# Kernel tuning notes

Measured on AMD Instinct MI355X. Metric: run time of the kernel, lower is better.

## Reference

```python
import jax, jax.numpy as jnp
import numpy as np

DIM = 192
NUM_HEADS = 6
KERNELS = [3, 5, 7]
DILATIONS = [1, 2, 3]
NBRANCH = 3
HEADS_B = NUM_HEADS // NBRANCH      # heads per branch = 2
HEAD_DIM = DIM // NUM_HEADS         # 32


def _axis_idx(L, K, d):
    """NATTEN-style neighborhood indices along one axis with dilation.
    Returns (nbr[L,K] absolute neighbor positions, bias[L,K] rpb indices in [0, 2K-2]).
    """
    i = np.arange(L)
    g = i % d                                 # dilation group
    ii = i // d                               # index within subgrid
    Lg = (L - g + d - 1) // d                 # subgrid length of each group
    start = np.clip(ii - K // 2, 0, Lg - K)   # clamp window inside bounds
    ki = np.arange(K)
    nbr = g[:, None] + (start[:, None] + ki[None, :]) * d        # [L,K]
    bias = start[:, None] + ki[None, :] - ii[:, None] + (K - 1)  # [L,K]
    return nbr, bias


def _branch(xb, K, d, rpb):
    # xb: [B,H,W, 3*heads*head_dim] laid out as (3, heads, head_dim)
    B, H, W, _ = xb.shape
    qkv = xb.reshape(B, H, W, 3, HEADS_B, HEAD_DIM).transpose(3, 0, 4, 1, 2, 5)
    q, k, v = qkv[0], qkv[1], qkv[2]          # [B,h,H,W,hd]
    q = q * (HEAD_DIM ** -0.5)
    nh, bh = _axis_idx(H, K, d)
    nw, bw = _axis_idx(W, K, d)
    # gather K x K neighborhoods: [B,h,H,W,K,K,hd]
    k_nb = k[:, :, nh[:, None, :, None], nw[None, :, None, :]]
    attn = jnp.einsum('bhijd,bhijkld->bhijkl', q, k_nb)
    attn = attn + rpb[:, bh[:, None, :, None], bw[None, :, None, :]][None]
    attn = jax.nn.softmax(attn.reshape(B, HEADS_B, H, W, K * K), axis=-1)
    attn = attn.reshape(B, HEADS_B, H, W, K, K)
    v_nb = v[:, :, nh[:, None, :, None], nw[None, :, None, :]]
    y = jnp.einsum('bhijkl,bhijkld->bhijd', attn, v_nb)
    return y.transpose(0, 2, 3, 1, 4).reshape(B, H, W, HEADS_B * HEAD_DIM)


def setup_inputs() -> dict:
    key = jax.random.key(0)
    ks = jax.random.split(key, 8)
    B, H, W = 8, 64, 64
    return {
        'x': jax.random.normal(ks[0], (B, DIM, H, W), jnp.float32),
        'qkv_w': jax.random.normal(ks[1], (3 * DIM, DIM), jnp.float32) * 0.02,
        'qkv_b': jnp.zeros((3 * DIM,), jnp.float32),
        'proj_w': jax.random.normal(ks[2], (DIM, DIM), jnp.float32) * 0.02,
        'proj_b': jnp.zeros((DIM,), jnp.float32),
        'rpb0': jax.random.normal(ks[3], (HEADS_B, 5, 5), jnp.float32) * 0.02,
        'rpb1': jax.random.normal(ks[4], (HEADS_B, 9, 9), jnp.float32) * 0.02,
        'rpb2': jax.random.normal(ks[5], (HEADS_B, 13, 13), jnp.float32) * 0.02,
    }


def reference(x, qkv_w, qkv_b, proj_w, proj_b, rpb0, rpb1, rpb2):
    # x: [B,C,H,W] -> BHWC
    xp = x.transpose(0, 2, 3, 1)
    qkv = xp @ qkv_w.T + qkv_b                 # [B,H,W,3*dim]
    branches = jnp.split(qkv, NBRANCH, axis=-1)  # equal channels (dim divisible by k)
    rpbs = [rpb0, rpb1, rpb2]
    ys = [_branch(branches[i], KERNELS[i], DILATIONS[i], rpbs[i]) for i in range(NBRANCH)]
    out = jnp.concatenate(ys, axis=-1) @ proj_w.T + proj_b
    return out.transpose(0, 3, 1, 2)
```

## Files before the change

### kernel.cpp

```cpp
#include <hip/hip_runtime.h>
#include <stdint.h>

typedef __attribute__((ext_vector_type(4))) float f32x4;
typedef _Float16 half8 __attribute__((ext_vector_type(8)));
typedef _Float16 half2v __attribute__((ext_vector_type(2)));

#define LDK 200
#define QSCALE 0.17677669529663689f

__device__ __forceinline__ float dot2f(unsigned int k2, unsigned int q2, float c) {
#if __has_builtin(__builtin_amdgcn_fdot2)
  return __builtin_amdgcn_fdot2(__builtin_bit_cast(half2v, k2),
                                __builtin_bit_cast(half2v, q2), c, false);
#else
  half2v a = __builtin_bit_cast(half2v, k2), b = __builtin_bit_cast(half2v, q2);
  return c + (float)a.x * (float)b.x + (float)a.y * (float)b.y;
#endif
}

#define MFMA16(A, B, C) __builtin_amdgcn_mfma_f32_16x16x32_f16(A, B, C, 0, 0, 0)

#define GLDS16(gsrc, ldst)                                                      \
  __builtin_amdgcn_global_load_lds(                                             \
      (const __attribute__((address_space(1))) void*)(gsrc),                    \
      (__attribute__((address_space(3))) void*)(ldst), 16, 0, 0)

__global__ __launch_bounds__(256) void prep(
    const float* __restrict__ x, const float* __restrict__ qw,
    const float* __restrict__ qb, const float* __restrict__ pw,
    _Float16* __restrict__ xh, _Float16* __restrict__ qwh,
    float* __restrict__ qbs, _Float16* __restrict__ pwh) {
  __shared__ __align__(16) _Float16 T[64 * LDK];
  const int bx = blockIdx.x, t = threadIdx.x;
  if (bx < 512) {
    const int bb = bx >> 6, hw0 = (bx & 63) << 6;
    const float* xb = x + (size_t)bb * 192 * 4096 + hw0;
    #pragma unroll
    for (int j = 0; j < 12; ++j) {
      int idx = j * 256 + t;
      int m4 = (idx & 15) * 4, c = idx >> 4;
      float4 v = *(const float4*)(xb + (size_t)c * 4096 + m4);
      T[(m4 + 0) * LDK + c] = (_Float16)v.x;
      T[(m4 + 1) * LDK + c] = (_Float16)v.y;
      T[(m4 + 2) * LDK + c] = (_Float16)v.z;
      T[(m4 + 3) * LDK + c] = (_Float16)v.w;
    }
    __syncthreads();
    _Float16* xo = xh + ((size_t)bb * 4096 + hw0) * 192;
    #pragma unroll
    for (int j = 0; j < 6; ++j) {
      int idx = j * 256 + t;
      int m = idx / 24, k8 = (idx % 24) * 8;
      *(uint4*)(xo + m * 192 + k8) = *(const uint4*)&T[m * LDK + k8];
    }
  } else {
    int i = (bx - 512) * 256 + t;
    if (i < 13824) {
      int n = i / 24, c = i % 24;
      const float* s = qw + n * 192 + c * 8;
      float sc = ((n % 192) < 64) ? QSCALE : 1.0f;
      half8 h = {(_Float16)(s[0] * sc), (_Float16)(s[1] * sc),
                 (_Float16)(s[2] * sc), (_Float16)(s[3] * sc),
                 (_Float16)(s[4] * sc), (_Float16)(s[5] * sc),
                 (_Float16)(s[6] * sc), (_Float16)(s[7] * sc)};
      *(half8*)(qwh + n * 192 + ((c ^ (n & 7)) << 3)) = h;
    } else if (i < 18432) {
      int k = i - 13824;
      int n = k / 24, c = k % 24;
      const float* s = pw + n * 192 + c * 8;
      half8 h = {(_Float16)s[0], (_Float16)s[1], (_Float16)s[2], (_Float16)s[3],
                 (_Float16)s[4], (_Float16)s[5], (_Float16)s[6], (_Float16)s[7]};
      *(half8*)(pwh + n * 192 + ((c ^ (n & 7)) << 3)) = h;
    } else if (i < 19008) {
      int n = i - 18432;
      qbs[n] = qb[n] * (((n % 192) < 64) ? QSCALE : 1.0f);
    }
  }
}

__global__ __launch_bounds__(256) void qkv_gemm(
    const _Float16* __restrict__ xh, const _Float16* __restrict__ wh,
    const float* __restrict__ qbs, _Float16* __restrict__ qkv) {
  __shared__ __align__(16) _Float16 Al[64 * LDK];
  __shared__ __align__(16) _Float16 Bsw[2][64 * 192];
  const int t = threadIdx.x;
  const int tm = blockIdx.x;
  const int lane = t & 63, wid = t >> 6;
  const int wm = (wid >> 1) * 32, wn = (wid & 1) * 32;
  const int lr = lane & 15, hi = lane >> 4;
  const int kb = hi * 8, r0 = hi * 4;
  const int xr = lr & 7;

  #pragma unroll
  for (int i = 0; i < 6; ++i)
    GLDS16(wh + (wid * 6 + i) * 512 + lane * 8, &Bsw[0][(wid * 6 + i) * 512]);

  {
    const _Float16* asrc = xh + (size_t)(tm * 64) * 192;
    uint4 av[6];
    #pragma unroll
    for (int q = 0; q < 6; ++q) av[q] = *(const uint4*)(asrc + (q * 256 + t) * 8);
    #pragma unroll
    for (int q = 0; q < 6; ++q) {
      int id = q * 256 + t;
      *(uint4*)&Al[(id / 24) * LDK + (id % 24) * 8] = av[q];
    }
  }
  __syncthreads();

  _Float16* opb = qkv + (size_t)(tm * 64) * 576;
  for (int it = 0; it < 9; ++it) {
    if (it < 8) {
      const _Float16* wsrc = wh + (it + 1) * 12288;
      _Float16* bdst = &Bsw[(it + 1) & 1][0];
      #pragma unroll
      for (int i = 0; i < 6; ++i)
        GLDS16(wsrc + (wid * 6 + i) * 512 + lane * 8, bdst + (wid * 6 + i) * 512);
    }
    const _Float16* bc = &Bsw[it & 1][0];

    f32x4 acc[2][2];
    #pragma unroll
    for (int i2 = 0; i2 < 2; ++i2)
      #pragma unroll
      for (int j = 0; j < 2; ++j)
        #pragma unroll
        for (int r = 0; r < 4; ++r) acc[i2][j][r] = 0.0f;

    #pragma unroll
    for (int k6 = 0; k6 < 6; ++k6) {
      half8 a0 = *(const half8*)&Al[(wm + lr) * LDK + k6 * 32 + kb];
      half8 a1 = *(const half8*)&Al[(wm + 16 + lr) * LDK + k6 * 32 + kb];
      const int cs = ((k6 * 4 + hi) ^ xr) << 3;
      half8 b0 = *(const half8*)&bc[(wn + lr) * 192 + cs];
      half8 b1 = *(const half8*)&bc[(wn + 16 + lr) * 192 + cs];
      acc[0][0] = MFMA16(a0, b0, acc[0][0]);
      acc[0][1] = MFMA16(a0, b1, acc[0][1]);
      acc[1][0] = MFMA16(a1, b0, acc[1][0]);
      acc[1][1] = MFMA16(a1, b1, acc[1][1]);
    }

    const int n0 = it * 64;
    const float bs0 = qbs[n0 + wn + lr], bs1 = qbs[n0 + wn + 16 + lr];
    #pragma unroll
    for (int i2 = 0; i2 < 2; ++i2)
      #pragma unroll
      for (int j = 0; j < 2; ++j) {
        int col = n0 + wn + j * 16 + lr;
        float bs = j ? bs1 : bs0;
        #pragma unroll
        for (int r = 0; r < 4; ++r)
          opb[(wm + i2 * 16 + r0 + r) * 576 + col] = (_Float16)(acc[i2][j][r] + bs);
      }
    __syncthreads();
  }
}

template <int K, int DIL>
__device__ __forceinline__ void natten_branch(
    const _Float16* __restrict__ qkv, const float* __restrict__ rpb,
    _Float16* __restrict__ yo, const int branch, const int r,
    unsigned short* __restrict__ smem) {
  constexpr int RW = 2 * K - 1;
  constexpr int H8 = K + 7;
  constexpr int NH = H8 * H8;
  constexpr int NL = (K * K + 3) / 4;
  constexpr int LSTR = 40;

  _Float16* Kl = (_Float16*)smem;
  _Float16* Vl = Kl + NH * LSTR;
  _Float16* Ql = Vl + NH * LSTR;
  float* rs = (float*)(Ql + 64 * LSTR);

  const int t = threadIdx.x;
  const int bh = r & 15;
  const int head = bh & 1, bb = bh >> 1;
  const int rr = r >> 4;
  int gh, gw, ti, tj, Lgh, Lgw;
  if (DIL == 1) {
    gh = 0; gw = 0; ti = (rr >> 3) * 8; tj = (rr & 7) * 8; Lgh = 64; Lgw = 64;
  } else if (DIL == 2) {
    int cls = rr >> 4, tile = rr & 15;
    gh = cls >> 1; gw = cls & 1; ti = (tile >> 2) * 8; tj = (tile & 3) * 8;
    Lgh = 32; Lgw = 32;
  } else {
    int cls = rr / 9, tile = rr % 9;
    gh = cls / 3; gw = cls % 3; ti = (tile / 3) * 8; tj = (tile % 3) * 8;
    Lgh = (64 - gh + 2) / 3; Lgw = (64 - gw + 2) / 3;
  }
  const int hoh = max(0, min(ti - K / 2, Lgh - K));
  const int how = max(0, min(tj - K / 2, Lgw - K));

  for (int i = t; i < RW * RW; i += 256) rs[i] = rpb[head * RW * RW + i];

  const _Float16* kvb = qkv + (size_t)bb * 4096 * 576 + branch * 192 + 64 + head * 32;
  for (int L = t; L < NH * 8; L += 256) {
    int px = L >> 3, part = L & 7;
    int hr = px / H8, hc = px % H8;
    int cr = min(hoh + hr, Lgh - 1), cc = min(how + hc, Lgw - 1);
    int ph = gh + cr * DIL, pw2 = gw + cc * DIL;
    const _Float16* src = kvb + (size_t)(ph * 64 + pw2) * 576 + (part & 3) * 8 + ((part & 4) ? 64 : 0);
    _Float16* dst = ((part & 4) ? Vl : Kl) + px * LSTR + (part & 3) * 8;
    *(uint4*)dst = *(const uint4*)src;
  }
  {
    int qi = t >> 2, part = t & 3;
    int ci0 = min(ti + (qi >> 3), Lgh - 1), cj0 = min(tj + (qi & 7), Lgw - 1);
    int ph = gh + ci0 * DIL, pw2 = gw + cj0 * DIL;
    const _Float16* src = qkv + (size_t)((size_t)bb * 4096 + ph * 64 + pw2) * 576
                          + branch * 192 + head * 32 + part * 8;
    *(uint4*)(Ql + qi * LSTR + part * 8) = *(const uint4*)src;
  }
  __syncthreads();

  const int qi = t >> 2, sl = t & 3;
  const int ci = ti + (qi >> 3), cj = tj + (qi & 7);
  const bool valid = (ci < Lgh) && (cj < Lgw);

  int s0h = ci - K / 2; if (s0h < 0) s0h = 0; if (s0h > Lgh - K) s0h = Lgh - K;
  int s0w = cj - K / 2; if (s0w < 0) s0w = 0; if (s0w > Lgw - K) s0w = Lgw - K;
  const int rbase = s0h - hoh, cbase = s0w - how;
  const int bhb = s0h - ci + K - 1, bwb = s0w - cj + K - 1;

  unsigned int qh[16];
  #pragma unroll
  for (int u = 0; u < 4; ++u) {
    uint4 v = *(const uint4*)(Ql + qi * LSTR + u * 8);
    qh[u * 4 + 0] = v.x; qh[u * 4 + 1] = v.y; qh[u * 4 + 2] = v.z; qh[u * 4 + 3] = v.w;
  }

  float s[NL];
  float mx = -1e30f;
  #pragma unroll
  for (int j = 0; j < NL; ++j) {
    int n = sl + 4 * j;
    if (n < K * K) {
      int kh = n / K, kw = n % K;
      int lidx = (rbase + kh) * H8 + (cbase + kw);
      const _Float16* kp = Kl + lidx * LSTR;
      float sc = rs[(bhb + kh) * RW + (bwb + kw)];
      #pragma unroll
      for (int u = 0; u < 4; ++u) {
        uint4 kv = *(const uint4*)(kp + u * 8);
        sc = dot2f(kv.x, qh[4 * u + 0], sc);
        sc = dot2f(kv.y, qh[4 * u + 1], sc);
        sc = dot2f(kv.z, qh[4 * u + 2], sc);
        sc = dot2f(kv.w, qh[4 * u + 3], sc);
      }
      s[j] = sc;
      mx = fmaxf(mx, sc);
    } else {
      s[j] = -1e30f;
    }
  }
  mx = fmaxf(mx, __shfl_xor(mx, 1, 64));
  mx = fmaxf(mx, __shfl_xor(mx, 2, 64));

  float pw[NL];
  float l = 0.0f;
  #pragma unroll
  for (int j = 0; j < NL; ++j) { pw[j] = __expf(s[j] - mx); l += pw[j]; }
  l += __shfl_xor(l, 1, 64);
  l += __shfl_xor(l, 2, 64);

  half2v acch[16];
  #pragma unroll
  for (int i = 0; i < 16; ++i) acch[i] = (half2v)(_Float16)0.0f;
  #pragma unroll
  for (int j = 0; j < NL; ++j) {
    int n = sl + 4 * j;
    if (n < K * K) {
      int kh = n / K, kw = n % K;
      int lidx = (rbase + kh) * H8 + (cbase + kw);
      const _Float16* vp = Vl + lidx * LSTR;
      _Float16 ph = (_Float16)pw[j];
      half2v pp = {ph, ph};
      #pragma unroll
      for (int u = 0; u < 4; ++u) {
        uint4 vv = *(const uint4*)(vp + u * 8);
        acch[4 * u + 0] += pp * __builtin_bit_cast(half2v, vv.x);
        acch[4 * u + 1] += pp * __builtin_bit_cast(half2v, vv.y);
        acch[4 * u + 2] += pp * __builtin_bit_cast(half2v, vv.z);
        acch[4 * u + 3] += pp * __builtin_bit_cast(half2v, vv.w);
      }
    }
  }
  #pragma unroll
  for (int st = 1; st <= 2; st <<= 1) {
    #pragma unroll
    for (int i = 0; i < 16; ++i) {
      unsigned int o = __shfl_xor(__builtin_bit_cast(unsigned int, acch[i]), st, 64);
      acch[i] += __builtin_bit_cast(half2v, o);
    }
  }

  if (valid) {
    float inv = 1.0f / l;
    _Float16 ih = (_Float16)inv;
    half2v iv = {ih, ih};
    unsigned int a[16];
    #pragma unroll
    for (int i = 0; i < 16; ++i) a[i] = __builtin_bit_cast(unsigned int, acch[i]);
    uint4 pk;
    unsigned int r0, r1, r2, r3;
    r0 = (sl < 2) ? ((sl == 0) ? a[0] : a[4]) : ((sl == 2) ? a[8] : a[12]);
    r1 = (sl < 2) ? ((sl == 0) ? a[1] : a[5]) : ((sl == 2) ? a[9] : a[13]);
    r2 = (sl < 2) ? ((sl == 0) ? a[2] : a[6]) : ((sl == 2) ? a[10] : a[14]);
    r3 = (sl < 2) ? ((sl == 0) ? a[3] : a[7]) : ((sl == 2) ? a[11] : a[15]);
    pk.x = __builtin_bit_cast(unsigned int, __builtin_bit_cast(half2v, r0) * iv);
    pk.y = __builtin_bit_cast(unsigned int, __builtin_bit_cast(half2v, r1) * iv);
    pk.z = __builtin_bit_cast(unsigned int, __builtin_bit_cast(half2v, r2) * iv);
    pk.w = __builtin_bit_cast(unsigned int, __builtin_bit_cast(half2v, r3) * iv);
    const int p = bb * 4096 + (gh + ci * DIL) * 64 + (gw + cj * DIL);
    *(uint4*)(yo + (size_t)p * 192 + branch * 64 + head * 32 + sl * 8) = pk;
  }
}

__global__ __launch_bounds__(256) void natten_all(
    const _Float16* __restrict__ qkv,
    const float* __restrict__ rpb0, const float* __restrict__ rpb1,
    const float* __restrict__ rpb2, _Float16* __restrict__ yo) {
  __shared__ __align__(16) unsigned short smem[18624];
  const int gid = blockIdx.x;
  if (gid < 1296)       natten_branch<7, 3>(qkv, rpb2, yo, 2, gid, smem);
  else if (gid < 2320)  natten_branch<5, 2>(qkv, rpb1, yo, 1, gid - 1296, smem);
  else                  natten_branch<3, 1>(qkv, rpb0, yo, 0, gid - 2320, smem);
}

__global__ __launch_bounds__(256) void proj_gemm(
    const _Float16* __restrict__ y, const _Float16* __restrict__ wh,
    const float* __restrict__ bias, float* __restrict__ out) {
  __shared__ __align__(16) _Float16 Bl[64 * LDK];
  __shared__ __align__(16) _Float16 Wsw[64 * 192];
  const int t = threadIdx.x;
  const int tp = blockIdx.x, c0 = blockIdx.y << 6;
  const int lane = t & 63, wid = t >> 6;
  const int wm = (wid >> 1) * 32, wn = (wid & 1) * 32;
  const int lr = lane & 15, hi = lane >> 4;
  const int kb = hi * 8, r0 = hi * 4;
  const int xr = lr & 7;

  #pragma unroll
  for (int i = 0; i < 6; ++i)
    GLDS16(wh + (size_t)c0 * 192 + (wid * 6 + i) * 512 + lane * 8,
           &Wsw[(wid * 6 + i) * 512]);

  {
    const _Float16* ysrc = y + (size_t)(tp * 64) * 192;
    uint4 yv[6];
    #pragma unroll
    for (int q = 0; q < 6; ++q) yv[q] = *(const uint4*)(ysrc + (q * 256 + t) * 8);
    #pragma unroll
    for (int q = 0; q < 6; ++q) {
      int id = q * 256 + t;
      *(uint4*)&Bl[(id / 24) * LDK + (id % 24) * 8] = yv[q];
    }
  }
  __syncthreads();

  f32x4 acc[2][2];
  #pragma unroll
  for (int i2 = 0; i2 < 2; ++i2)
    #pragma unroll
    for (int j = 0; j < 2; ++j)
      #pragma unroll
      for (int r = 0; r < 4; ++r) acc[i2][j][r] = 0.0f;

  #pragma unroll
  for (int k6 = 0; k6 < 6; ++k6) {
    const int cs = ((k6 * 4 + hi) ^ xr) << 3;
    half8 a0 = *(const half8*)&Wsw[(wm + lr) * 192 + cs];
    half8 a1 = *(const half8*)&Wsw[(wm + 16 + lr) * 192 + cs];
    half8 b0 = *(const half8*)&Bl[(wn + lr) * LDK + k6 * 32 + kb];
    half8 b1 = *(const half8*)&Bl[(wn + 16 + lr) * LDK + k6 * 32 + kb];
    acc[0][0] = MFMA16(a0, b0, acc[0][0]);
    acc[0][1] = MFMA16(a0, b1, acc[0][1]);
    acc[1][0] = MFMA16(a1, b0, acc[1][0]);
    acc[1][1] = MFMA16(a1, b1, acc[1][1]);
  }

  const int gp = tp * 64;
  const int bb = gp >> 12, hw0 = gp & 4095;
  float* op = out + (size_t)bb * 192 * 4096 + hw0;
  #pragma unroll
  for (int i2 = 0; i2 < 2; ++i2)
    #pragma unroll
    for (int j = 0; j < 2; ++j) {
      int m = wn + j * 16 + lr;
      #pragma unroll
      for (int r = 0; r < 4; ++r) {
        int c = c0 + wm + i2 * 16 + r0 + r;
        op[(size_t)c * 4096 + m] = acc[i2][j][r] + bias[c];
      }
    }
}

extern "C" void kernel_launch(void* const* d_in, const int* in_sizes, int n_in,
                              void* d_out, int out_size, void* d_ws, size_t ws_size,
                              hipStream_t stream) {
  const float* x      = (const float*)d_in[0];
  const float* qkv_w  = (const float*)d_in[1];
  const float* qkv_b  = (const float*)d_in[2];
  const float* proj_w = (const float*)d_in[3];
  const float* proj_b = (const float*)d_in[4];
  const float* rpb0   = (const float*)d_in[5];
  const float* rpb1   = (const float*)d_in[6];
  const float* rpb2   = (const float*)d_in[7];

  _Float16* qkv = (_Float16*)d_ws;
  _Float16* yb  = qkv + (size_t)32768 * 576;
  _Float16* xh  = yb + (size_t)32768 * 192;
  _Float16* qwh = xh + (size_t)32768 * 192;
  _Float16* pwh = qwh + 110592;
  float*    qbs = (float*)(pwh + 36864);
  float* out = (float*)d_out;

  prep<<<dim3(587), 256, 0, stream>>>(x, qkv_w, qkv_b, proj_w, xh, qwh, qbs, pwh);
  qkv_gemm<<<dim3(512), 256, 0, stream>>>(xh, qwh, qbs, qkv);
  natten_all<<<dim3(3344), 256, 0, stream>>>(qkv, rpb0, rpb1, rpb2, yb);
  proj_gemm<<<dim3(512, 3), 256, 0, stream>>>(yb, pwh, proj_b, out);
}
```

Baseline: 140.3 us.

## Fuse input transpose into QKV GEMM, loop proj over channel tiles, unroll gather

```diff
diff --git a/kernel.cpp b/kernel.cpp
--- a/kernel.cpp
+++ b/kernel.cpp
@@ -26,60 +26,34 @@
       (__attribute__((address_space(3))) void*)(ldst), 16, 0, 0)
 
 __global__ __launch_bounds__(256) void prep(
-    const float* __restrict__ x, const float* __restrict__ qw,
-    const float* __restrict__ qb, const float* __restrict__ pw,
-    _Float16* __restrict__ xh, _Float16* __restrict__ qwh,
-    float* __restrict__ qbs, _Float16* __restrict__ pwh) {
-  __shared__ __align__(16) _Float16 T[64 * LDK];
-  const int bx = blockIdx.x, t = threadIdx.x;
-  if (bx < 512) {
-    const int bb = bx >> 6, hw0 = (bx & 63) << 6;
-    const float* xb = x + (size_t)bb * 192 * 4096 + hw0;
-    #pragma unroll
-    for (int j = 0; j < 12; ++j) {
-      int idx = j * 256 + t;
-      int m4 = (idx & 15) * 4, c = idx >> 4;
-      float4 v = *(const float4*)(xb + (size_t)c * 4096 + m4);
-      T[(m4 + 0) * LDK + c] = (_Float16)v.x;
-      T[(m4 + 1) * LDK + c] = (_Float16)v.y;
-      T[(m4 + 2) * LDK + c] = (_Float16)v.z;
-      T[(m4 + 3) * LDK + c] = (_Float16)v.w;
-    }
-    __syncthreads();
-    _Float16* xo = xh + ((size_t)bb * 4096 + hw0) * 192;
-    #pragma unroll
-    for (int j = 0; j < 6; ++j) {
-      int idx = j * 256 + t;
-      int m = idx / 24, k8 = (idx % 24) * 8;
-      *(uint4*)(xo + m * 192 + k8) = *(const uint4*)&T[m * LDK + k8];
-    }
-  } else {
-    int i = (bx - 512) * 256 + t;
-    if (i < 13824) {
-      int n = i / 24, c = i % 24;
-      const float* s = qw + n * 192 + c * 8;
-      float sc = ((n % 192) < 64) ? QSCALE : 1.0f;
-      half8 h = {(_Float16)(s[0] * sc), (_Float16)(s[1] * sc),
-                 (_Float16)(s[2] * sc), (_Float16)(s[3] * sc),
-                 (_Float16)(s[4] * sc), (_Float16)(s[5] * sc),
-                 (_Float16)(s[6] * sc), (_Float16)(s[7] * sc)};
-      *(half8*)(qwh + n * 192 + ((c ^ (n & 7)) << 3)) = h;
-    } else if (i < 18432) {
-      int k = i - 13824;
-      int n = k / 24, c = k % 24;
-      const float* s = pw + n * 192 + c * 8;
-      half8 h = {(_Float16)s[0], (_Float16)s[1], (_Float16)s[2], (_Float16)s[3],
-                 (_Float16)s[4], (_Float16)s[5], (_Float16)s[6], (_Float16)s[7]};
-      *(half8*)(pwh + n * 192 + ((c ^ (n & 7)) << 3)) = h;
-    } else if (i < 19008) {
-      int n = i - 18432;
-      qbs[n] = qb[n] * (((n % 192) < 64) ? QSCALE : 1.0f);
-    }
+    const float* __restrict__ qw, const float* __restrict__ qb,
+    const float* __restrict__ pw,
+    _Float16* __restrict__ qwh, float* __restrict__ qbs, _Float16* __restrict__ pwh) {
+  int i = blockIdx.x * 256 + threadIdx.x;
+  if (i < 13824) {
+    int n = i / 24, c = i % 24;
+    const float* s = qw + n * 192 + c * 8;
+    float sc = ((n % 192) < 64) ? QSCALE : 1.0f;
+    half8 h = {(_Float16)(s[0] * sc), (_Float16)(s[1] * sc),
+               (_Float16)(s[2] * sc), (_Float16)(s[3] * sc),
+               (_Float16)(s[4] * sc), (_Float16)(s[5] * sc),
+               (_Float16)(s[6] * sc), (_Float16)(s[7] * sc)};
+    *(half8*)(qwh + n * 192 + ((c ^ (n & 7)) << 3)) = h;
+  } else if (i < 18432) {
+    int k = i - 13824;
+    int n = k / 24, c = k % 24;
+    const float* s = pw + n * 192 + c * 8;
+    half8 h = {(_Float16)s[0], (_Float16)s[1], (_Float16)s[2], (_Float16)s[3],
+               (_Float16)s[4], (_Float16)s[5], (_Float16)s[6], (_Float16)s[7]};
+    *(half8*)(pwh + n * 192 + ((c ^ (n & 7)) << 3)) = h;
+  } else if (i < 19008) {
+    int n = i - 18432;
+    qbs[n] = qb[n] * (((n % 192) < 64) ? QSCALE : 1.0f);
   }
 }
 
 __global__ __launch_bounds__(256) void qkv_gemm(
-    const _Float16* __restrict__ xh, const _Float16* __restrict__ wh,
+    const float* __restrict__ x, const _Float16* __restrict__ wh,
     const float* __restrict__ qbs, _Float16* __restrict__ qkv) {
   __shared__ __align__(16) _Float16 Al[64 * LDK];
   __shared__ __align__(16) _Float16 Bsw[2][64 * 192];
@@ -96,14 +70,17 @@
     GLDS16(wh + (wid * 6 + i) * 512 + lane * 8, &Bsw[0][(wid * 6 + i) * 512]);
 
   {
-    const _Float16* asrc = xh + (size_t)(tm * 64) * 192;
-    uint4 av[6];
-    #pragma unroll
-    for (int q = 0; q < 6; ++q) av[q] = *(const uint4*)(asrc + (q * 256 + t) * 8);
-    #pragma unroll
-    for (int q = 0; q < 6; ++q) {
-      int id = q * 256 + t;
-      *(uint4*)&Al[(id / 24) * LDK + (id % 24) * 8] = av[q];
+    const int bb = tm >> 6, hw0 = (tm & 63) << 6;
+    const float* xb = x + (size_t)bb * 192 * 4096 + hw0;
+    #pragma unroll
+    for (int j = 0; j < 12; ++j) {
+      int idx = j * 256 + t;
+      int m4 = (idx & 15) * 4, c = idx >> 4;
+      float4 v = *(const float4*)(xb + (size_t)c * 4096 + m4);
+      Al[(m4 + 0) * LDK + c] = (_Float16)v.x;
+      Al[(m4 + 1) * LDK + c] = (_Float16)v.y;
+      Al[(m4 + 2) * LDK + c] = (_Float16)v.z;
+      Al[(m4 + 3) * LDK + c] = (_Float16)v.w;
     }
   }
   __syncthreads();
@@ -166,6 +143,8 @@
   constexpr int NH = H8 * H8;
   constexpr int NL = (K * K + 3) / 4;
   constexpr int LSTR = 40;
+  constexpr int NITER = (NH * 8 + 255) / 256;
+  constexpr int DH = 32 / H8, DC = 32 % H8;
 
   _Float16* Kl = (_Float16*)smem;
   _Float16* Vl = Kl + NH * LSTR;
@@ -193,15 +172,24 @@
 
   for (int i = t; i < RW * RW; i += 256) rs[i] = rpb[head * RW * RW + i];
 
-  const _Float16* kvb = qkv + (size_t)bb * 4096 * 576 + branch * 192 + 64 + head * 32;
-  for (int L = t; L < NH * 8; L += 256) {
-    int px = L >> 3, part = L & 7;
-    int hr = px / H8, hc = px % H8;
-    int cr = min(hoh + hr, Lgh - 1), cc = min(how + hc, Lgw - 1);
-    int ph = gh + cr * DIL, pw2 = gw + cc * DIL;
-    const _Float16* src = kvb + (size_t)(ph * 64 + pw2) * 576 + (part & 3) * 8 + ((part & 4) ? 64 : 0);
-    _Float16* dst = ((part & 4) ? Vl : Kl) + px * LSTR + (part & 3) * 8;
-    *(uint4*)dst = *(const uint4*)src;
+  {
+    const _Float16* kvb = qkv + (size_t)bb * 4096 * 576 + branch * 192 + 64 + head * 32;
+    const int part = t & 7;
+    const int coff = (part & 3) * 8;
+    const _Float16* gsrc = kvb + coff + ((part & 4) ? 64 : 0);
+    _Float16* dbase = ((part & 4) ? Vl : Kl) + coff;
+    int px = t >> 3;
+    int hr = px / H8, hc = px - hr * H8;
+    #pragma unroll
+    for (int itn = 0; itn < NITER; ++itn) {
+      if (px < NH) {
+        int cr = min(hoh + hr, Lgh - 1), cc = min(how + hc, Lgw - 1);
+        int ph = gh + cr * DIL, pw2 = gw + cc * DIL;
+        *(uint4*)(dbase + px * LSTR) = *(const uint4*)(gsrc + (size_t)(ph * 64 + pw2) * 576);
+      }
+      px += 32; hr += DH; hc += DC;
+      if (hc >= H8) { hc -= H8; ++hr; }
+    }
   }
   {
     int qi = t >> 2, part = t & 3;
@@ -331,9 +319,9 @@
     const _Float16* __restrict__ y, const _Float16* __restrict__ wh,
     const float* __restrict__ bias, float* __restrict__ out) {
   __shared__ __align__(16) _Float16 Bl[64 * LDK];
-  __shared__ __align__(16) _Float16 Wsw[64 * 192];
+  __shared__ __align__(16) _Float16 Wsw[2][64 * 192];
   const int t = threadIdx.x;
-  const int tp = blockIdx.x, c0 = blockIdx.y << 6;
+  const int tp = blockIdx.x;
   const int lane = t & 63, wid = t >> 6;
   const int wm = (wid >> 1) * 32, wn = (wid & 1) * 32;
   const int lr = lane & 15, hi = lane >> 4;
@@ -342,8 +330,7 @@
 
   #pragma unroll
   for (int i = 0; i < 6; ++i)
-    GLDS16(wh + (size_t)c0 * 192 + (wid * 6 + i) * 512 + lane * 8,
-           &Wsw[(wid * 6 + i) * 512]);
+    GLDS16(wh + (wid * 6 + i) * 512 + lane * 8, &Wsw[0][(wid * 6 + i) * 512]);
 
   {
     const _Float16* ysrc = y + (size_t)(tp * 64) * 192;
@@ -358,41 +345,55 @@
   }
   __syncthreads();
 
-  f32x4 acc[2][2];
-  #pragma unroll
-  for (int i2 = 0; i2 < 2; ++i2)
-    #pragma unroll
-    for (int j = 0; j < 2; ++j)
-      #pragma unroll
-      for (int r = 0; r < 4; ++r) acc[i2][j][r] = 0.0f;
-
-  #pragma unroll
-  for (int k6 = 0; k6 < 6; ++k6) {
-    const int cs = ((k6 * 4 + hi) ^ xr) << 3;
-    half8 a0 = *(const half8*)&Wsw[(wm + lr) * 192 + cs];
-    half8 a1 = *(const half8*)&Wsw[(wm + 16 + lr) * 192 + cs];
-    half8 b0 = *(const half8*)&Bl[(wn + lr) * LDK + k6 * 32 + kb];
-    half8 b1 = *(const half8*)&Bl[(wn + 16 + lr) * LDK + k6 * 32 + kb];
-    acc[0][0] = MFMA16(a0, b0, acc[0][0]);
-    acc[0][1] = MFMA16(a0, b1, acc[0][1]);
-    acc[1][0] = MFMA16(a1, b0, acc[1][0]);
-    acc[1][1] = MFMA16(a1, b1, acc[1][1]);
-  }
-
   const int gp = tp * 64;
   const int bb = gp >> 12, hw0 = gp & 4095;
   float* op = out + (size_t)bb * 192 * 4096 + hw0;
-  #pragma unroll
-  for (int i2 = 0; i2 < 2; ++i2)
-    #pragma unroll
-    for (int j = 0; j < 2; ++j) {
-      int m = wn + j * 16 + lr;
-      #pragma unroll
-      for (int r = 0; r < 4; ++r) {
-        int c = c0 + wm + i2 * 16 + r0 + r;
-        op[(size_t)c * 4096 + m] = acc[i2][j][r] + bias[c];
+
+  for (int ci = 0; ci < 3; ++ci) {
+    if (ci < 2) {
+      const _Float16* wsrc = wh + (ci + 1) * 12288;
+      _Float16* wdst = &Wsw[(ci + 1) & 1][0];
+      #pragma unroll
+      for (int i = 0; i < 6; ++i)
+        GLDS16(wsrc + (wid * 6 + i) * 512 + lane * 8, wdst + (wid * 6 + i) * 512);
+    }
+    const _Float16* wc = &Wsw[ci & 1][0];
+
+    f32x4 acc[2][2];
+    #pragma unroll
+    for (int i2 = 0; i2 < 2; ++i2)
+      #pragma unroll
+      for (int j = 0; j < 2; ++j)
+        #pragma unroll
+        for (int r = 0; r < 4; ++r) acc[i2][j][r] = 0.0f;
+
+    #pragma unroll
+    for (int k6 = 0; k6 < 6; ++k6) {
+      const int cs = ((k6 * 4 + hi) ^ xr) << 3;
+      half8 a0 = *(const half8*)&wc[(wm + lr) * 192 + cs];
+      half8 a1 = *(const half8*)&wc[(wm + 16 + lr) * 192 + cs];
+      half8 b0 = *(const half8*)&Bl[(wn + lr) * LDK + k6 * 32 + kb];
+      half8 b1 = *(const half8*)&Bl[(wn + 16 + lr) * LDK + k6 * 32 + kb];
+      acc[0][0] = MFMA16(a0, b0, acc[0][0]);
+      acc[0][1] = MFMA16(a0, b1, acc[0][1]);
+      acc[1][0] = MFMA16(a1, b0, acc[1][0]);
+      acc[1][1] = MFMA16(a1, b1, acc[1][1]);
+    }
+
+    const int c0 = ci << 6;
+    #pragma unroll
+    for (int i2 = 0; i2 < 2; ++i2)
+      #pragma unroll
+      for (int j = 0; j < 2; ++j) {
+        int m = wn + j * 16 + lr;
+        #pragma unroll
+        for (int r = 0; r < 4; ++r) {
+          int c = c0 + wm + i2 * 16 + r0 + r;
+          op[(size_t)c * 4096 + m] = acc[i2][j][r] + bias[c];
+        }
       }
-    }
+    __syncthreads();
+  }
 }
 
 extern "C" void kernel_launch(void* const* d_in, const int* in_sizes, int n_in,
@@ -409,14 +410,13 @@
 
   _Float16* qkv = (_Float16*)d_ws;
   _Float16* yb  = qkv + (size_t)32768 * 576;
-  _Float16* xh  = yb + (size_t)32768 * 192;
-  _Float16* qwh = xh + (size_t)32768 * 192;
+  _Float16* qwh = yb + (size_t)32768 * 192;
   _Float16* pwh = qwh + 110592;
   float*    qbs = (float*)(pwh + 36864);
   float* out = (float*)d_out;
 
-  prep<<<dim3(587), 256, 0, stream>>>(x, qkv_w, qkv_b, proj_w, xh, qwh, qbs, pwh);
-  qkv_gemm<<<dim3(512), 256, 0, stream>>>(xh, qwh, qbs, qkv);
+  prep<<<dim3(75), 256, 0, stream>>>(qkv_w, qkv_b, proj_w, qwh, qbs, pwh);
+  qkv_gemm<<<dim3(512), 256, 0, stream>>>(x, qwh, qbs, qkv);
   natten_all<<<dim3(3344), 256, 0, stream>>>(qkv, rpb0, rpb1, rpb2, yb);
-  proj_gemm<<<dim3(512, 3), 256, 0, stream>>>(yb, pwh, proj_b, out);
-}
+  proj_gemm<<<dim3(512), 256, 0, stream>>>(yb, pwh, proj_b, out);
+}
```

After: 135.6 us. 3.4% less time.
